# Kernel optimization log

Measured on AMD Instinct MI355X. Metric: run time of the kernel, lower is better.

## Reference

```python
import jax, jax.numpy as jnp
import numpy as np
from jax import lax

# QuantumDMRGLayer (isolated_labelnode=True) as a pure MPS chain contraction.
# Per sample: contract each site's (2,m[,m]) tensor with the 2-dim input vector
# over the physical leg, then multiply the resulting bond matrices along the
# chain, inserting the (m,m,nblabels) output tensor after site pos_label.

B, L, M, NBL = 2048, 196, 16, 10  # batch, dimvec, bond_len, nblabels


def setup_inputs() -> dict:
    key = jax.random.key(0)
    k_in, k_mid, k_l, k_r, k_out = jax.random.split(key, 5)
    # std chosen for numerical stability of a 196-long matrix product:
    # each site matrix is x0*A[0]+x1*A[1] with x~N(0,1), so effective per-site
    # gain ~ std*sqrt(2*m); std = 1/sqrt(2*m) keeps the product O(1).
    std = 1.0 / np.sqrt(2.0 * M)
    inputs = jax.random.normal(k_in, (B, L, 2), dtype=jnp.float32)
    eye2m = jnp.eye(M, dtype=jnp.float32)[:2, :]  # eye(max(2,m))[0:2,:] -> (2, m)
    A_left = eye2m + 1e-3 * jax.random.normal(k_l, (2, M), dtype=jnp.float32)
    A_right = eye2m + 1e-3 * jax.random.normal(k_r, (2, M), dtype=jnp.float32)
    A_mid = std * jax.random.normal(k_mid, (L - 2, 2, M, M), dtype=jnp.float32)
    T_out = (1.0 / np.sqrt(M)) * jax.random.normal(k_out, (M, M, NBL), dtype=jnp.float32)
    return {
        "inputs": inputs,
        "A_left": A_left,
        "A_mid": A_mid,
        "A_right": A_right,
        "T_out": T_out,
        "pos_label": 98,
    }


def reference(inputs, A_left, A_mid, A_right, T_out, pos_label):
    # Contract physical legs: interior site i (1..L-2) -> batched (m,m) matrix.
    mats = jnp.einsum("bsd,sdij->sbij", inputs[:, 1:-1, :], A_mid)  # (L-2, B, m, m)
    v_left = jnp.einsum("bd,dm->bm", inputs[:, 0, :], A_left)       # (B, m)
    v_right = jnp.einsum("bd,dm->bm", inputs[:, -1, :], A_right)    # (B, m)

    def step_l(v, Mx):  # v @ M, batched
        return jnp.einsum("bm,bmn->bn", v, Mx), None

    def step_r(v, Mx):  # M @ v, batched (sweep from the right end inward)
        return jnp.einsum("bmn,bn->bm", Mx, v), None

    # sites 1..pos_label feed the left bond of the output node,
    # sites pos_label+1..L-2 feed the right bond.
    left, _ = lax.scan(step_l, v_left, mats[:pos_label])
    right, _ = lax.scan(step_r, v_right, mats[pos_label:], reverse=True)
    return jnp.einsum("bm,mnl,bn->bl", left, T_out, right)  # (B, nblabels)
```

## Files before the change

kernel.cpp:

```cpp
#include <hip/hip_runtime.h>


typedef __attribute__((ext_vector_type(8))) short short8;
typedef __attribute__((ext_vector_type(16))) float floatx16;

#define PSET_DW 512
#define PAIR_DW (2 * PSET_DW)
#define LSTEPS 49
#define RSTEPS 48
#define RBASE_DW (LSTEPS * PAIR_DW)
#define WST_OFF_DW ((LSTEPS + RSTEPS) * PAIR_DW)

__device__ __forceinline__ unsigned bf16_rne(unsigned u) {
    return (u + 0x7FFFu + ((u >> 16) & 1u)) >> 16;
}

__global__ __launch_bounds__(256)
void prep_pair(const float* __restrict__ AM, unsigned* __restrict__ WS)
{
    __shared__ float sA0[2][16][16];
    __shared__ float sA1[2][16][16];
    const int pidx = blockIdx.x;
    const int tid  = threadIdx.x;
    const int dir  = (pidx >= LSTEPS) ? 1 : 0;
    const int t    = dir ? (pidx - LSTEPS) : pidx;
    const int a0   = dir ? (192 - 2 * t) : (2 * t);
    const int a1   = a0 + 1;

    for (int i = tid; i < 512; i += 256) {
        ((float*)sA0)[i] = AM[a0 * 512 + i];
        ((float*)sA1)[i] = AM[a1 * 512 + i];
    }
    __syncthreads();

    unsigned* gp = WS + (dir ? (RBASE_DW + t * PAIR_DW) : (t * PAIR_DW));
    for (int u = tid; u < 512; u += 256) {
        const int s_   = u >> 8;
        const int lane = (u & 255) >> 2;
        const int w_   = u & 3;
        const int r    = lane & 31;
        const int kb   = (lane >> 5) << 3;
        const int d    = r >> 4;
        const int rl   = r & 15;
        const int sig  = (rl & 3) | ((rl & 4) << 1) | ((rl & 8) >> 1);
        const int b0 = s_, b1 = d;
        const int k0 = kb + 2 * w_;
        float q0 = 0.f, q1 = 0.f;
        if (dir == 0) {
#pragma unroll
            for (int m_ = 0; m_ < 16; ++m_) {
                const float a1v = sA1[b1][m_][sig];
                q0 = fmaf(sA0[b0][k0][m_],     a1v, q0);
                q1 = fmaf(sA0[b0][k0 + 1][m_], a1v, q1);
            }
        } else {
#pragma unroll
            for (int m_ = 0; m_ < 16; ++m_) {
                const float a0v = sA0[b0][sig][m_];
                q0 = fmaf(a0v, sA1[b1][m_][k0],     q0);
                q1 = fmaf(a0v, sA1[b1][m_][k0 + 1], q1);
            }
        }
        const unsigned u0 = __float_as_uint(q0), u1 = __float_as_uint(q1);
        const unsigned h0 = bf16_rne(u0), h1 = bf16_rne(u1);
        const float l0f = q0 - __uint_as_float(h0 << 16);
        const float l1f = q1 - __uint_as_float(h1 << 16);
        const unsigned lo0 = bf16_rne(__float_as_uint(l0f));
        const unsigned lo1 = bf16_rne(__float_as_uint(l1f));
        gp[s_ * PSET_DW + lane * 4 + w_]       = (h1 << 16) | h0;
        gp[s_ * PSET_DW + 256 + lane * 4 + w_] = (lo1 << 16) | lo0;
    }
}

__global__ __launch_bounds__(64, 1)
void chain_kernel(const float* __restrict__ X,
                  const float* __restrict__ AL,
                  const float* __restrict__ AR,
                  const unsigned* __restrict__ WS,
                  float* __restrict__ WST)
{
    const int lane = threadIdx.x;
    const int dir  = blockIdx.x & 1;
    const int s    = (blockIdx.x >> 1) * 32 + (lane & 31);
    const int kb   = (lane >> 5) << 3;
    const float* Xs = X + s * 392;
    const unsigned* Gb = WS + (dir ? RBASE_DW : 0) + lane * 4;
    const int nsteps = dir ? RSTEPS : LSTEPS;

    float w[8];
    int4 vh4, vl4;
    auto pack = [&]() {
#pragma unroll
        for (int q = 0; q < 4; ++q) {
            const unsigned u0 = __float_as_uint(w[2 * q]);
            const unsigned u1 = __float_as_uint(w[2 * q + 1]);
            const unsigned h0 = u0 & 0xFFFF0000u, h1 = u1 & 0xFFFF0000u;
            const float l0 = w[2 * q]     - __uint_as_float(h0);
            const float l1 = w[2 * q + 1] - __uint_as_float(h1);
            ((unsigned*)&vh4)[q] = h1 | (h0 >> 16);
            ((unsigned*)&vl4)[q] = (__float_as_uint(l1) & 0xFFFF0000u) |
                                   (__float_as_uint(l0) >> 16);
        }
    };

    const float* Ai = dir ? AR : AL;
    const float2 xi = *(const float2*)(Xs + (dir ? 390 : 0));
#pragma unroll
    for (int j = 0; j < 8; ++j)
        w[j] = xi.x * Ai[kb + j] + xi.y * Ai[16 + kb + j];
    pack();

    const floatx16 Z = {};

    int4 GH0[2], GL0[2], GH1[2], GL1[2];
    float2 xp[2], xq[2];
    {
        const unsigned* gp0 = Gb;
        GH0[0] = *(const int4*)(gp0);
        GL0[0] = *(const int4*)(gp0 + 256);
        GH1[0] = *(const int4*)(gp0 + PSET_DW);
        GL1[0] = *(const int4*)(gp0 + PSET_DW + 256);
        const int xo0 = dir ? 386 : 2;
        xp[0] = *(const float2*)(Xs + xo0);
        xq[0] = *(const float2*)(Xs + xo0 + 2);
        const unsigned* gp1 = Gb + PAIR_DW;
        GH0[1] = *(const int4*)(gp1);
        GL0[1] = *(const int4*)(gp1 + 256);
        GH1[1] = *(const int4*)(gp1 + PSET_DW);
        GL1[1] = *(const int4*)(gp1 + PSET_DW + 256);
        const int xo1 = dir ? 382 : 6;
        xp[1] = *(const float2*)(Xs + xo1);
        xq[1] = *(const float2*)(Xs + xo1 + 2);
    }

    for (int c = 0; c < 25; ++c) {
#pragma unroll
        for (int half = 0; half < 2; ++half) {
            const int t = 2 * c + half;
            if (t < nsteps) {
                const short8 ah0 = *(const short8*)&GH0[half];
                const short8 al0 = *(const short8*)&GL0[half];
                const short8 ah1 = *(const short8*)&GH1[half];
                const short8 al1 = *(const short8*)&GL1[half];
                const float2 xpc = xp[half], xqc = xq[half];

                const int tn = (t + 2 < nsteps) ? (t + 2) : t;
                const unsigned* gp = Gb + tn * PAIR_DW;
                GH0[half] = *(const int4*)(gp);
                GL0[half] = *(const int4*)(gp + 256);
                GH1[half] = *(const int4*)(gp + PSET_DW);
                GL1[half] = *(const int4*)(gp + PSET_DW + 256);
                const int xo = dir ? (386 - 4 * tn) : (4 * tn + 2);
                xp[half] = *(const float2*)(Xs + xo);
                xq[half] = *(const float2*)(Xs + xo + 2);

                const short8 bh = *(const short8*)&vh4;
                const short8 bl = *(const short8*)&vl4;
                floatx16 D0, D1;
                D0 = __builtin_amdgcn_mfma_f32_32x32x16_bf16(ah0, bh, Z,  0, 0, 0);
                D1 = __builtin_amdgcn_mfma_f32_32x32x16_bf16(ah1, bh, Z,  0, 0, 0);
                D0 = __builtin_amdgcn_mfma_f32_32x32x16_bf16(ah0, bl, D0, 0, 0, 0);
                D1 = __builtin_amdgcn_mfma_f32_32x32x16_bf16(ah1, bl, D1, 0, 0, 0);
                D0 = __builtin_amdgcn_mfma_f32_32x32x16_bf16(al0, bh, D0, 0, 0, 0);
                D1 = __builtin_amdgcn_mfma_f32_32x32x16_bf16(al1, bh, D1, 0, 0, 0);

                const float c0 = xpc.x * xqc.x, c1 = xpc.x * xqc.y;
                const float c2 = xpc.y * xqc.x, c3 = xpc.y * xqc.y;
#pragma unroll
                for (int j = 0; j < 8; ++j)
                    w[j] = fmaf(c0, D0[j],
                           fmaf(c1, D0[j + 8],
                           fmaf(c2, D1[j], c3 * D1[j + 8])));
                pack();
            }
        }
    }

    float* st = WST + (dir * 2048 + s) * 16 + kb;
    *(float4*)(st)     = make_float4(w[0], w[1], w[2], w[3]);
    *(float4*)(st + 4) = make_float4(w[4], w[5], w[6], w[7]);
}

__global__ __launch_bounds__(256)
void out_kernel(const float* __restrict__ T, const float* __restrict__ WST,
                float* __restrict__ OUT)
{
    __shared__ float sT[2560];
    const int tid = threadIdx.x;
    for (int k = tid; k < 640; k += 256)
        ((float4*)sT)[k] = ((const float4*)T)[k];
    __syncthreads();
    const int t = blockIdx.x * 256 + tid;
    const int s = t / 10, l = t - s * 10;
    const float* L = WST + s * 16;
    const float* R = WST + 2048 * 16 + s * 16;
    const float4 Ra = *(const float4*)(R);
    const float4 Rb = *(const float4*)(R + 4);
    const float4 Rc = *(const float4*)(R + 8);
    const float4 Rd = *(const float4*)(R + 12);
    float acc = 0.f;
#pragma unroll
    for (int m = 0; m < 16; ++m) {
        const float lm = L[m];
        const float* Tp = sT + m * 160 + l;
        acc = fmaf(lm * Ra.x, Tp[0],   acc);
        acc = fmaf(lm * Ra.y, Tp[10],  acc);
        acc = fmaf(lm * Ra.z, Tp[20],  acc);
        acc = fmaf(lm * Ra.w, Tp[30],  acc);
        acc = fmaf(lm * Rb.x, Tp[40],  acc);
        acc = fmaf(lm * Rb.y, Tp[50],  acc);
        acc = fmaf(lm * Rb.z, Tp[60],  acc);
        acc = fmaf(lm * Rb.w, Tp[70],  acc);
        acc = fmaf(lm * Rc.x, Tp[80],  acc);
        acc = fmaf(lm * Rc.y, Tp[90],  acc);
        acc = fmaf(lm * Rc.z, Tp[100], acc);
        acc = fmaf(lm * Rc.w, Tp[110], acc);
        acc = fmaf(lm * Rd.x, Tp[120], acc);
        acc = fmaf(lm * Rd.y, Tp[130], acc);
        acc = fmaf(lm * Rd.z, Tp[140], acc);
        acc = fmaf(lm * Rd.w, Tp[150], acc);
    }
    OUT[t] = acc;
}

extern "C" void kernel_launch(void* const* d_in, const int* in_sizes, int n_in,
                              void* d_out, int out_size, void* d_ws, size_t ws_size,
                              hipStream_t stream)
{
    const float* X  = (const float*)d_in[0];
    const float* AL = (const float*)d_in[1];
    const float* AM = (const float*)d_in[2];
    const float* AR = (const float*)d_in[3];
    const float* T  = (const float*)d_in[4];
    (void)in_sizes; (void)n_in; (void)out_size; (void)ws_size;
    unsigned* WS = (unsigned*)d_ws;
    float* WST   = (float*)d_ws + WST_OFF_DW;
    float* OUT   = (float*)d_out;

    hipLaunchKernelGGL(prep_pair,    dim3(97),  dim3(256), 0, stream, AM, WS);
    hipLaunchKernelGGL(chain_kernel, dim3(128), dim3(64),  0, stream,
                       X, AL, AR, WS, WST);
    hipLaunchKernelGGL(out_kernel,   dim3(80),  dim3(256), 0, stream,
                       T, WST, OUT);
}
```

Measured before the change: 85.54 us.

## Fuse prep, chain and output kernels into one cooperative kernel with grid syncs

Merges the three launches (pair-product prep, MFMA chain sweep, output contraction) into a single cooperative kernel of 128 blocks of 256 threads, separated by two grid-wide syncs. The goal is to remove the per-launch overhead and inter-kernel gaps. In exchange it adds grid.sync costs, and the chain phase now runs only 64 of 256 threads per block, so the other three wavefronts sit idle.

```diff
diff --git a/kernel.cpp b/kernel.cpp
--- a/kernel.cpp
+++ b/kernel.cpp
@@ -1,5 +1,8 @@
 #include <hip/hip_runtime.h>
-
+#include <hip/hip_cooperative_groups.h>
+
+
+namespace cg = cooperative_groups;
 
 typedef __attribute__((ext_vector_type(8))) short short8;
 typedef __attribute__((ext_vector_type(16))) float floatx16;
@@ -15,212 +18,223 @@
     return (u + 0x7FFFu + ((u >> 16) & 1u)) >> 16;
 }
 
-__global__ __launch_bounds__(256)
-void prep_pair(const float* __restrict__ AM, unsigned* __restrict__ WS)
+#define PACK(W, VH, VL)                                                      \
+    {                                                                        \
+        _Pragma("unroll")                                                    \
+        for (int q = 0; q < 4; ++q) {                                        \
+            const unsigned u0 = __float_as_uint(W[2 * q]);                   \
+            const unsigned u1 = __float_as_uint(W[2 * q + 1]);               \
+            const unsigned h0 = u0 & 0xFFFF0000u, h1 = u1 & 0xFFFF0000u;     \
+            const float l0 = W[2 * q]     - __uint_as_float(h0);             \
+            const float l1 = W[2 * q + 1] - __uint_as_float(h1);             \
+            ((unsigned*)&VH)[q] = h1 | (h0 >> 16);                           \
+            ((unsigned*)&VL)[q] = (__float_as_uint(l1) & 0xFFFF0000u) |      \
+                                  (__float_as_uint(l0) >> 16);               \
+        }                                                                    \
+    }
+
+__global__ __launch_bounds__(256, 1)
+void mega_kernel(const float* __restrict__ X,
+                 const float* __restrict__ AL,
+                 const float* __restrict__ AR,
+                 const float* __restrict__ AM,
+                 const float* __restrict__ T,
+                 unsigned* __restrict__ WS,
+                 float* __restrict__ WST,
+                 float* __restrict__ OUT)
 {
+    cg::grid_group grid = cg::this_grid();
+
     __shared__ float sA0[2][16][16];
     __shared__ float sA1[2][16][16];
-    const int pidx = blockIdx.x;
-    const int tid  = threadIdx.x;
-    const int dir  = (pidx >= LSTEPS) ? 1 : 0;
-    const int t    = dir ? (pidx - LSTEPS) : pidx;
-    const int a0   = dir ? (192 - 2 * t) : (2 * t);
-    const int a1   = a0 + 1;
-
-    for (int i = tid; i < 512; i += 256) {
-        ((float*)sA0)[i] = AM[a0 * 512 + i];
-        ((float*)sA1)[i] = AM[a1 * 512 + i];
-    }
-    __syncthreads();
-
-    unsigned* gp = WS + (dir ? (RBASE_DW + t * PAIR_DW) : (t * PAIR_DW));
-    for (int u = tid; u < 512; u += 256) {
-        const int s_   = u >> 8;
-        const int lane = (u & 255) >> 2;
-        const int w_   = u & 3;
-        const int r    = lane & 31;
+    __shared__ float sT[2560];
+
+    const int tid = threadIdx.x;
+    const int bid = blockIdx.x;
+
+    if (bid < 97) {
+        const int dir = (bid >= LSTEPS) ? 1 : 0;
+        const int t   = dir ? (bid - LSTEPS) : bid;
+        const int a0  = dir ? (192 - 2 * t) : (2 * t);
+        const int a1  = a0 + 1;
+
+        for (int i = tid; i < 512; i += 256) {
+            ((float*)sA0)[i] = AM[a0 * 512 + i];
+            ((float*)sA1)[i] = AM[a1 * 512 + i];
+        }
+        __syncthreads();
+
+        unsigned* gp = WS + (dir ? (RBASE_DW + t * PAIR_DW) : (t * PAIR_DW));
+        for (int u = tid; u < 512; u += 256) {
+            const int s_   = u >> 8;
+            const int lane = (u & 255) >> 2;
+            const int w_   = u & 3;
+            const int r    = lane & 31;
+            const int kb   = (lane >> 5) << 3;
+            const int d    = r >> 4;
+            const int rl   = r & 15;
+            const int sig  = (rl & 3) | ((rl & 4) << 1) | ((rl & 8) >> 1);
+            const int b0 = s_, b1 = d;
+            const int k0 = kb + 2 * w_;
+            float q0 = 0.f, q1 = 0.f;
+            if (dir == 0) {
+#pragma unroll
+                for (int m_ = 0; m_ < 16; ++m_) {
+                    const float a1v = sA1[b1][m_][sig];
+                    q0 = fmaf(sA0[b0][k0][m_],     a1v, q0);
+                    q1 = fmaf(sA0[b0][k0 + 1][m_], a1v, q1);
+                }
+            } else {
+#pragma unroll
+                for (int m_ = 0; m_ < 16; ++m_) {
+                    const float a0v = sA0[b0][sig][m_];
+                    q0 = fmaf(a0v, sA1[b1][m_][k0],     q0);
+                    q1 = fmaf(a0v, sA1[b1][m_][k0 + 1], q1);
+                }
+            }
+            const unsigned u0 = __float_as_uint(q0), u1 = __float_as_uint(q1);
+            const unsigned h0 = bf16_rne(u0), h1 = bf16_rne(u1);
+            const float l0f = q0 - __uint_as_float(h0 << 16);
+            const float l1f = q1 - __uint_as_float(h1 << 16);
+            const unsigned lo0 = bf16_rne(__float_as_uint(l0f));
+            const unsigned lo1 = bf16_rne(__float_as_uint(l1f));
+            gp[s_ * PSET_DW + lane * 4 + w_]       = (h1 << 16) | h0;
+            gp[s_ * PSET_DW + 256 + lane * 4 + w_] = (lo1 << 16) | lo0;
+        }
+    }
+
+    grid.sync();
+
+    if (tid < 64) {
+        const int lane = tid;
+        const int dir  = bid & 1;
+        const int s    = (bid >> 1) * 32 + (lane & 31);
         const int kb   = (lane >> 5) << 3;
-        const int d    = r >> 4;
-        const int rl   = r & 15;
-        const int sig  = (rl & 3) | ((rl & 4) << 1) | ((rl & 8) >> 1);
-        const int b0 = s_, b1 = d;
-        const int k0 = kb + 2 * w_;
-        float q0 = 0.f, q1 = 0.f;
-        if (dir == 0) {
-#pragma unroll
-            for (int m_ = 0; m_ < 16; ++m_) {
-                const float a1v = sA1[b1][m_][sig];
-                q0 = fmaf(sA0[b0][k0][m_],     a1v, q0);
-                q1 = fmaf(sA0[b0][k0 + 1][m_], a1v, q1);
+        const float* Xs = X + s * 392;
+        const unsigned* Gb = WS + (dir ? RBASE_DW : 0) + lane * 4;
+        const int nsteps = dir ? RSTEPS : LSTEPS;
+
+        float w[8];
+        int4 vh4, vl4;
+
+        const float* Ai = dir ? AR : AL;
+        const float2 xi = *(const float2*)(Xs + (dir ? 390 : 0));
+#pragma unroll
+        for (int j = 0; j < 8; ++j)
+            w[j] = xi.x * Ai[kb + j] + xi.y * Ai[16 + kb + j];
+        PACK(w, vh4, vl4);
+
+        const floatx16 Z = {};
+
+        int4 GH0[2], GL0[2], GH1[2], GL1[2];
+        float2 xp[2], xq[2];
+        {
+            const unsigned* gp0 = Gb;
+            GH0[0] = *(const int4*)(gp0);
+            GL0[0] = *(const int4*)(gp0 + 256);
+            GH1[0] = *(const int4*)(gp0 + PSET_DW);
+            GL1[0] = *(const int4*)(gp0 + PSET_DW + 256);
+            const int xo0 = dir ? 386 : 2;
+            xp[0] = *(const float2*)(Xs + xo0);
+            xq[0] = *(const float2*)(Xs + xo0 + 2);
+            const unsigned* gp1 = Gb + PAIR_DW;
+            GH0[1] = *(const int4*)(gp1);
+            GL0[1] = *(const int4*)(gp1 + 256);
+            GH1[1] = *(const int4*)(gp1 + PSET_DW);
+            GL1[1] = *(const int4*)(gp1 + PSET_DW + 256);
+            const int xo1 = dir ? 382 : 6;
+            xp[1] = *(const float2*)(Xs + xo1);
+            xq[1] = *(const float2*)(Xs + xo1 + 2);
+        }
+
+        for (int c = 0; c < 25; ++c) {
+#pragma unroll
+            for (int half = 0; half < 2; ++half) {
+                const int t = 2 * c + half;
+                if (t < nsteps) {
+                    const short8 ah0 = *(const short8*)&GH0[half];
+                    const short8 al0 = *(const short8*)&GL0[half];
+                    const short8 ah1 = *(const short8*)&GH1[half];
+                    const short8 al1 = *(const short8*)&GL1[half];
+                    const float2 xpc = xp[half], xqc = xq[half];
+
+                    const int tn = (t + 2 < nsteps) ? (t + 2) : t;
+                    const unsigned* gp = Gb + tn * PAIR_DW;
+                    GH0[half] = *(const int4*)(gp);
+                    GL0[half] = *(const int4*)(gp + 256);
+                    GH1[half] = *(const int4*)(gp + PSET_DW);
+                    GL1[half] = *(const int4*)(gp + PSET_DW + 256);
+                    const int xo = dir ? (386 - 4 * tn) : (4 * tn + 2);
+                    xp[half] = *(const float2*)(Xs + xo);
+                    xq[half] = *(const float2*)(Xs + xo + 2);
+
+                    const short8 bh = *(const short8*)&vh4;
+                    const short8 bl = *(const short8*)&vl4;
+                    floatx16 D0, D1;
+                    D0 = __builtin_amdgcn_mfma_f32_32x32x16_bf16(ah0, bh, Z,  0, 0, 0);
+                    D1 = __builtin_amdgcn_mfma_f32_32x32x16_bf16(ah1, bh, Z,  0, 0, 0);
+                    D0 = __builtin_amdgcn_mfma_f32_32x32x16_bf16(ah0, bl, D0, 0, 0, 0);
+                    D1 = __builtin_amdgcn_mfma_f32_32x32x16_bf16(ah1, bl, D1, 0, 0, 0);
+                    D0 = __builtin_amdgcn_mfma_f32_32x32x16_bf16(al0, bh, D0, 0, 0, 0);
+                    D1 = __builtin_amdgcn_mfma_f32_32x32x16_bf16(al1, bh, D1, 0, 0, 0);
+
+                    const float c0 = xpc.x * xqc.x, c1 = xpc.x * xqc.y;
+                    const float c2 = xpc.y * xqc.x, c3 = xpc.y * xqc.y;
+#pragma unroll
+                    for (int j = 0; j < 8; ++j)
+                        w[j] = fmaf(c0, D0[j],
+                               fmaf(c1, D0[j + 8],
+                               fmaf(c2, D1[j], c3 * D1[j + 8])));
+                    PACK(w, vh4, vl4);
+                }
             }
-        } else {
-#pragma unroll
-            for (int m_ = 0; m_ < 16; ++m_) {
-                const float a0v = sA0[b0][sig][m_];
-                q0 = fmaf(a0v, sA1[b1][m_][k0],     q0);
-                q1 = fmaf(a0v, sA1[b1][m_][k0 + 1], q1);
-            }
-        }
-        const unsigned u0 = __float_as_uint(q0), u1 = __float_as_uint(q1);
-        const unsigned h0 = bf16_rne(u0), h1 = bf16_rne(u1);
-        const float l0f = q0 - __uint_as_float(h0 << 16);
-        const float l1f = q1 - __uint_as_float(h1 << 16);
-        const unsigned lo0 = bf16_rne(__float_as_uint(l0f));
-        const unsigned lo1 = bf16_rne(__float_as_uint(l1f));
-        gp[s_ * PSET_DW + lane * 4 + w_]       = (h1 << 16) | h0;
-        gp[s_ * PSET_DW + 256 + lane * 4 + w_] = (lo1 << 16) | lo0;
-    }
-}
-
-__global__ __launch_bounds__(64, 1)
-void chain_kernel(const float* __restrict__ X,
-                  const float* __restrict__ AL,
-                  const float* __restrict__ AR,
-                  const unsigned* __restrict__ WS,
-                  float* __restrict__ WST)
-{
-    const int lane = threadIdx.x;
-    const int dir  = blockIdx.x & 1;
-    const int s    = (blockIdx.x >> 1) * 32 + (lane & 31);
-    const int kb   = (lane >> 5) << 3;
-    const float* Xs = X + s * 392;
-    const unsigned* Gb = WS + (dir ? RBASE_DW : 0) + lane * 4;
-    const int nsteps = dir ? RSTEPS : LSTEPS;
-
-    float w[8];
-    int4 vh4, vl4;
-    auto pack = [&]() {
-#pragma unroll
-        for (int q = 0; q < 4; ++q) {
-            const unsigned u0 = __float_as_uint(w[2 * q]);
-            const unsigned u1 = __float_as_uint(w[2 * q + 1]);
-            const unsigned h0 = u0 & 0xFFFF0000u, h1 = u1 & 0xFFFF0000u;
-            const float l0 = w[2 * q]     - __uint_as_float(h0);
-            const float l1 = w[2 * q + 1] - __uint_as_float(h1);
-            ((unsigned*)&vh4)[q] = h1 | (h0 >> 16);
-            ((unsigned*)&vl4)[q] = (__float_as_uint(l1) & 0xFFFF0000u) |
-                                   (__float_as_uint(l0) >> 16);
-        }
-    };
-
-    const float* Ai = dir ? AR : AL;
-    const float2 xi = *(const float2*)(Xs + (dir ? 390 : 0));
-#pragma unroll
-    for (int j = 0; j < 8; ++j)
-        w[j] = xi.x * Ai[kb + j] + xi.y * Ai[16 + kb + j];
-    pack();
-
-    const floatx16 Z = {};
-
-    int4 GH0[2], GL0[2], GH1[2], GL1[2];
-    float2 xp[2], xq[2];
-    {
-        const unsigned* gp0 = Gb;
-        GH0[0] = *(const int4*)(gp0);
-        GL0[0] = *(const int4*)(gp0 + 256);
-        GH1[0] = *(const int4*)(gp0 + PSET_DW);
-        GL1[0] = *(const int4*)(gp0 + PSET_DW + 256);
-        const int xo0 = dir ? 386 : 2;
-        xp[0] = *(const float2*)(Xs + xo0);
-        xq[0] = *(const float2*)(Xs + xo0 + 2);
-        const unsigned* gp1 = Gb + PAIR_DW;
-        GH0[1] = *(const int4*)(gp1);
-        GL0[1] = *(const int4*)(gp1 + 256);
-        GH1[1] = *(const int4*)(gp1 + PSET_DW);
-        GL1[1] = *(const int4*)(gp1 + PSET_DW + 256);
-        const int xo1 = dir ? 382 : 6;
-        xp[1] = *(const float2*)(Xs + xo1);
-        xq[1] = *(const float2*)(Xs + xo1 + 2);
-    }
-
-    for (int c = 0; c < 25; ++c) {
-#pragma unroll
-        for (int half = 0; half < 2; ++half) {
-            const int t = 2 * c + half;
-            if (t < nsteps) {
-                const short8 ah0 = *(const short8*)&GH0[half];
-                const short8 al0 = *(const short8*)&GL0[half];
-                const short8 ah1 = *(const short8*)&GH1[half];
-                const short8 al1 = *(const short8*)&GL1[half];
-                const float2 xpc = xp[half], xqc = xq[half];
-
-                const int tn = (t + 2 < nsteps) ? (t + 2) : t;
-                const unsigned* gp = Gb + tn * PAIR_DW;
-                GH0[half] = *(const int4*)(gp);
-                GL0[half] = *(const int4*)(gp + 256);
-                GH1[half] = *(const int4*)(gp + PSET_DW);
-                GL1[half] = *(const int4*)(gp + PSET_DW + 256);
-                const int xo = dir ? (386 - 4 * tn) : (4 * tn + 2);
-                xp[half] = *(const float2*)(Xs + xo);
-                xq[half] = *(const float2*)(Xs + xo + 2);
-
-                const short8 bh = *(const short8*)&vh4;
-                const short8 bl = *(const short8*)&vl4;
-                floatx16 D0, D1;
-                D0 = __builtin_amdgcn_mfma_f32_32x32x16_bf16(ah0, bh, Z,  0, 0, 0);
-                D1 = __builtin_amdgcn_mfma_f32_32x32x16_bf16(ah1, bh, Z,  0, 0, 0);
-                D0 = __builtin_amdgcn_mfma_f32_32x32x16_bf16(ah0, bl, D0, 0, 0, 0);
-                D1 = __builtin_amdgcn_mfma_f32_32x32x16_bf16(ah1, bl, D1, 0, 0, 0);
-                D0 = __builtin_amdgcn_mfma_f32_32x32x16_bf16(al0, bh, D0, 0, 0, 0);
-                D1 = __builtin_amdgcn_mfma_f32_32x32x16_bf16(al1, bh, D1, 0, 0, 0);
-
-                const float c0 = xpc.x * xqc.x, c1 = xpc.x * xqc.y;
-                const float c2 = xpc.y * xqc.x, c3 = xpc.y * xqc.y;
-#pragma unroll
-                for (int j = 0; j < 8; ++j)
-                    w[j] = fmaf(c0, D0[j],
-                           fmaf(c1, D0[j + 8],
-                           fmaf(c2, D1[j], c3 * D1[j + 8])));
-                pack();
-            }
-        }
-    }
-
-    float* st = WST + (dir * 2048 + s) * 16 + kb;
-    *(float4*)(st)     = make_float4(w[0], w[1], w[2], w[3]);
-    *(float4*)(st + 4) = make_float4(w[4], w[5], w[6], w[7]);
-}
-
-__global__ __launch_bounds__(256)
-void out_kernel(const float* __restrict__ T, const float* __restrict__ WST,
-                float* __restrict__ OUT)
-{
-    __shared__ float sT[2560];
-    const int tid = threadIdx.x;
+        }
+
+        float* st = WST + (dir * 2048 + s) * 16 + kb;
+        *(float4*)(st)     = make_float4(w[0], w[1], w[2], w[3]);
+        *(float4*)(st + 4) = make_float4(w[4], w[5], w[6], w[7]);
+    }
+
     for (int k = tid; k < 640; k += 256)
         ((float4*)sT)[k] = ((const float4*)T)[k];
-    __syncthreads();
-    const int t = blockIdx.x * 256 + tid;
-    const int s = t / 10, l = t - s * 10;
-    const float* L = WST + s * 16;
-    const float* R = WST + 2048 * 16 + s * 16;
-    const float4 Ra = *(const float4*)(R);
-    const float4 Rb = *(const float4*)(R + 4);
-    const float4 Rc = *(const float4*)(R + 8);
-    const float4 Rd = *(const float4*)(R + 12);
-    float acc = 0.f;
-#pragma unroll
-    for (int m = 0; m < 16; ++m) {
-        const float lm = L[m];
-        const float* Tp = sT + m * 160 + l;
-        acc = fmaf(lm * Ra.x, Tp[0],   acc);
-        acc = fmaf(lm * Ra.y, Tp[10],  acc);
-        acc = fmaf(lm * Ra.z, Tp[20],  acc);
-        acc = fmaf(lm * Ra.w, Tp[30],  acc);
-        acc = fmaf(lm * Rb.x, Tp[40],  acc);
-        acc = fmaf(lm * Rb.y, Tp[50],  acc);
-        acc = fmaf(lm * Rb.z, Tp[60],  acc);
-        acc = fmaf(lm * Rb.w, Tp[70],  acc);
-        acc = fmaf(lm * Rc.x, Tp[80],  acc);
-        acc = fmaf(lm * Rc.y, Tp[90],  acc);
-        acc = fmaf(lm * Rc.z, Tp[100], acc);
-        acc = fmaf(lm * Rc.w, Tp[110], acc);
-        acc = fmaf(lm * Rd.x, Tp[120], acc);
-        acc = fmaf(lm * Rd.y, Tp[130], acc);
-        acc = fmaf(lm * Rd.z, Tp[140], acc);
-        acc = fmaf(lm * Rd.w, Tp[150], acc);
-    }
-    OUT[t] = acc;
+
+    grid.sync();
+
+    {
+        const int t = bid * 256 + tid;
+        if (t < 20480) {
+            const int s = t / 10, l = t - s * 10;
+            const float* L = WST + s * 16;
+            const float* R = WST + 2048 * 16 + s * 16;
+            const float4 Ra = *(const float4*)(R);
+            const float4 Rb = *(const float4*)(R + 4);
+            const float4 Rc = *(const float4*)(R + 8);
+            const float4 Rd = *(const float4*)(R + 12);
+            float acc = 0.f;
+#pragma unroll
+            for (int m = 0; m < 16; ++m) {
+                const float lm = L[m];
+                const float* Tp = sT + m * 160 + l;
+                acc = fmaf(lm * Ra.x, Tp[0],   acc);
+                acc = fmaf(lm * Ra.y, Tp[10],  acc);
+                acc = fmaf(lm * Ra.z, Tp[20],  acc);
+                acc = fmaf(lm * Ra.w, Tp[30],  acc);
+                acc = fmaf(lm * Rb.x, Tp[40],  acc);
+                acc = fmaf(lm * Rb.y, Tp[50],  acc);
+                acc = fmaf(lm * Rb.z, Tp[60],  acc);
+                acc = fmaf(lm * Rb.w, Tp[70],  acc);
+                acc = fmaf(lm * Rc.x, Tp[80],  acc);
+                acc = fmaf(lm * Rc.y, Tp[90],  acc);
+                acc = fmaf(lm * Rc.z, Tp[100], acc);
+                acc = fmaf(lm * Rc.w, Tp[110], acc);
+                acc = fmaf(lm * Rd.x, Tp[120], acc);
+                acc = fmaf(lm * Rd.y, Tp[130], acc);
+                acc = fmaf(lm * Rd.z, Tp[140], acc);
+                acc = fmaf(lm * Rd.w, Tp[150], acc);
+            }
+            OUT[t] = acc;
+        }
+    }
 }
 
 extern "C" void kernel_launch(void* const* d_in, const int* in_sizes, int n_in,
@@ -237,9 +251,8 @@
     float* WST   = (float*)d_ws + WST_OFF_DW;
     float* OUT   = (float*)d_out;
 
-    hipLaunchKernelGGL(prep_pair,    dim3(97),  dim3(256), 0, stream, AM, WS);
-    hipLaunchKernelGGL(chain_kernel, dim3(128), dim3(64),  0, stream,
-                       X, AL, AR, WS, WST);
-    hipLaunchKernelGGL(out_kernel,   dim3(80),  dim3(256), 0, stream,
-                       T, WST, OUT);
+    void* kargs[] = { (void*)&X, (void*)&AL, (void*)&AR, (void*)&AM,
+                      (void*)&T, (void*)&WS, (void*)&WST, (void*)&OUT };
+    hipLaunchCooperativeKernel((const void*)mega_kernel,
+                               dim3(128), dim3(256), kargs, 0, stream);
 }
```

New measurement: 134.8 us. 1.58x slower.

## Stream chain weights through an 8-deep LDS ring via global_load_lds

Applied to the files above, without the earlier changes.

The sequential chain loop used to prefetch each step's bf16 hi/lo weight fragments straight into registers, only two steps ahead. Now `global_load_lds` stages weights into an 8-slot shared-memory ring, eight steps ahead, and each step reads the next slot from LDS. The goal is to hide global-memory latency on this latency-bound serial chain behind a deeper prefetch. The cost is 32 KB of LDS, extra LDS reads, and hand-coded `s_waitcnt` vmcnt values that must match the X loads issued in the same loop. Any mismatch there would be a correctness hazard.

```diff
diff --git a/kernel.cpp b/kernel.cpp
--- a/kernel.cpp
+++ b/kernel.cpp
@@ -72,6 +72,28 @@
     }
 }
 
+#define PACK(W, VH, VL)                                                      \
+    {                                                                        \
+        _Pragma("unroll")                                                    \
+        for (int q = 0; q < 4; ++q) {                                        \
+            const unsigned u0 = __float_as_uint(W[2 * q]);                   \
+            const unsigned u1 = __float_as_uint(W[2 * q + 1]);               \
+            const unsigned h0 = u0 & 0xFFFF0000u, h1 = u1 & 0xFFFF0000u;     \
+            const float l0 = W[2 * q]     - __uint_as_float(h0);             \
+            const float l1 = W[2 * q + 1] - __uint_as_float(h1);             \
+            ((unsigned*)&VH)[q] = h1 | (h0 >> 16);                           \
+            ((unsigned*)&VL)[q] = (__float_as_uint(l1) & 0xFFFF0000u) |      \
+                                  (__float_as_uint(l0) >> 16);               \
+        }                                                                    \
+    }
+
+__device__ __forceinline__ void gload_lds16(const unsigned* g, unsigned* l)
+{
+    __builtin_amdgcn_global_load_lds(
+        (const __attribute__((address_space(1))) unsigned*)g,
+        (__attribute__((address_space(3))) unsigned*)l, 16, 0, 0);
+}
+
 __global__ __launch_bounds__(64, 1)
 void chain_kernel(const float* __restrict__ X,
                   const float* __restrict__ AL,
@@ -79,55 +101,56 @@
                   const unsigned* __restrict__ WS,
                   float* __restrict__ WST)
 {
+    __shared__ unsigned sG[8 * 1024] __attribute__((aligned(16)));
+
     const int lane = threadIdx.x;
     const int dir  = blockIdx.x & 1;
     const int s    = (blockIdx.x >> 1) * 32 + (lane & 31);
     const int kb   = (lane >> 5) << 3;
     const float* Xs = X + s * 392;
-    const unsigned* Gb = WS + (dir ? RBASE_DW : 0) + lane * 4;
+    const unsigned* Gdir = WS + (dir ? RBASE_DW : 0);
     const int nsteps = dir ? RSTEPS : LSTEPS;
+
+    auto stage = [&](int tn) {
+        const unsigned* gsb = Gdir + tn * PAIR_DW + lane * 4;
+        unsigned* lds = sG + (tn & 7) * 1024;
+        gload_lds16(gsb,       lds);
+        gload_lds16(gsb + 256, lds + 256);
+        gload_lds16(gsb + 512, lds + 512);
+        gload_lds16(gsb + 768, lds + 768);
+    };
+
+#pragma unroll
+    for (int i = 0; i < 8; ++i) stage(i);
+    __builtin_amdgcn_s_waitcnt(0x0F70);
+    __builtin_amdgcn_sched_barrier(0);
 
     float w[8];
     int4 vh4, vl4;
-    auto pack = [&]() {
-#pragma unroll
-        for (int q = 0; q < 4; ++q) {
-            const unsigned u0 = __float_as_uint(w[2 * q]);
-            const unsigned u1 = __float_as_uint(w[2 * q + 1]);
-            const unsigned h0 = u0 & 0xFFFF0000u, h1 = u1 & 0xFFFF0000u;
-            const float l0 = w[2 * q]     - __uint_as_float(h0);
-            const float l1 = w[2 * q + 1] - __uint_as_float(h1);
-            ((unsigned*)&vh4)[q] = h1 | (h0 >> 16);
-            ((unsigned*)&vl4)[q] = (__float_as_uint(l1) & 0xFFFF0000u) |
-                                   (__float_as_uint(l0) >> 16);
-        }
-    };
-
-    const float* Ai = dir ? AR : AL;
-    const float2 xi = *(const float2*)(Xs + (dir ? 390 : 0));
-#pragma unroll
-    for (int j = 0; j < 8; ++j)
-        w[j] = xi.x * Ai[kb + j] + xi.y * Ai[16 + kb + j];
-    pack();
+    {
+        const float* Ai = dir ? AR : AL;
+        const float2 xi = *(const float2*)(Xs + (dir ? 390 : 0));
+#pragma unroll
+        for (int j = 0; j < 8; ++j)
+            w[j] = xi.x * Ai[kb + j] + xi.y * Ai[16 + kb + j];
+        PACK(w, vh4, vl4);
+    }
 
     const floatx16 Z = {};
 
-    int4 GH0[2], GL0[2], GH1[2], GL1[2];
+    int4 GH0r[2], GL0r[2], GH1r[2], GL1r[2];
+    {
+        const int4* sp = (const int4*)(sG);
+        GH0r[0] = sp[lane];
+        GL0r[0] = sp[64 + lane];
+        GH1r[0] = sp[128 + lane];
+        GL1r[0] = sp[192 + lane];
+    }
     float2 xp[2], xq[2];
     {
-        const unsigned* gp0 = Gb;
-        GH0[0] = *(const int4*)(gp0);
-        GL0[0] = *(const int4*)(gp0 + 256);
-        GH1[0] = *(const int4*)(gp0 + PSET_DW);
-        GL1[0] = *(const int4*)(gp0 + PSET_DW + 256);
         const int xo0 = dir ? 386 : 2;
         xp[0] = *(const float2*)(Xs + xo0);
         xq[0] = *(const float2*)(Xs + xo0 + 2);
-        const unsigned* gp1 = Gb + PAIR_DW;
-        GH0[1] = *(const int4*)(gp1);
-        GL0[1] = *(const int4*)(gp1 + 256);
-        GH1[1] = *(const int4*)(gp1 + PSET_DW);
-        GL1[1] = *(const int4*)(gp1 + PSET_DW + 256);
         const int xo1 = dir ? 382 : 6;
         xp[1] = *(const float2*)(Xs + xo1);
         xq[1] = *(const float2*)(Xs + xo1 + 2);
@@ -137,22 +160,21 @@
 #pragma unroll
         for (int half = 0; half < 2; ++half) {
             const int t = 2 * c + half;
+            __builtin_amdgcn_s_waitcnt(0x0F76);
+            __builtin_amdgcn_sched_barrier(0);
+            {
+                const int4* sp = (const int4*)(sG + ((t + 1) & 7) * 1024);
+                GH0r[half ^ 1] = sp[lane];
+                GL0r[half ^ 1] = sp[64 + lane];
+                GH1r[half ^ 1] = sp[128 + lane];
+                GL1r[half ^ 1] = sp[192 + lane];
+            }
             if (t < nsteps) {
-                const short8 ah0 = *(const short8*)&GH0[half];
-                const short8 al0 = *(const short8*)&GL0[half];
-                const short8 ah1 = *(const short8*)&GH1[half];
-                const short8 al1 = *(const short8*)&GL1[half];
+                const short8 ah0 = *(const short8*)&GH0r[half];
+                const short8 al0 = *(const short8*)&GL0r[half];
+                const short8 ah1 = *(const short8*)&GH1r[half];
+                const short8 al1 = *(const short8*)&GL1r[half];
                 const float2 xpc = xp[half], xqc = xq[half];
-
-                const int tn = (t + 2 < nsteps) ? (t + 2) : t;
-                const unsigned* gp = Gb + tn * PAIR_DW;
-                GH0[half] = *(const int4*)(gp);
-                GL0[half] = *(const int4*)(gp + 256);
-                GH1[half] = *(const int4*)(gp + PSET_DW);
-                GL1[half] = *(const int4*)(gp + PSET_DW + 256);
-                const int xo = dir ? (386 - 4 * tn) : (4 * tn + 2);
-                xp[half] = *(const float2*)(Xs + xo);
-                xq[half] = *(const float2*)(Xs + xo + 2);
 
                 const short8 bh = *(const short8*)&vh4;
                 const short8 bl = *(const short8*)&vl4;
@@ -171,8 +193,15 @@
                     w[j] = fmaf(c0, D0[j],
                            fmaf(c1, D0[j + 8],
                            fmaf(c2, D1[j], c3 * D1[j + 8])));
-                pack();
-            }
+                PACK(w, vh4, vl4);
+
+                const int tn = (t + 2 < nsteps) ? (t + 2) : t;
+                const int xo = dir ? (386 - 4 * tn) : (4 * tn + 2);
+                xp[half] = *(const float2*)(Xs + xo);
+                xq[half] = *(const float2*)(Xs + xo + 2);
+            }
+            const int tn8 = (t + 8 < nsteps) ? (t + 8) : (nsteps - 1);
+            stage(tn8);
         }
     }
 
```

Result: slower. 87.96 us (+2.8%).
